# Performance work log

Measured on AMD Instinct MI355X. Metric: run time of the kernel, lower is better.

## Reference

```python
import jax, jax.numpy as jnp
import numpy as np


def setup_inputs() -> dict:
    key = jax.random.key(0)
    ks = jax.random.split(key, 6)
    B, C, H, W, Q = 16, 64, 64, 64, 8192
    HID = 256
    K = C * 9  # 576, unfolded channel count and srnet out_dim (co_mat=1)
    feat = jax.random.normal(ks[0], (B, C, H, W), jnp.float32)
    coord = jax.random.uniform(ks[1], (B, Q, 2), jnp.float32) * 2.0 - 1.0  # normalized [-1,1]
    cell = jnp.ones((B, Q, 2), jnp.float32) * (2.0 / 128.0)  # HR cell size for 128-px grid
    w1 = jax.random.normal(ks[2], (3, HID), jnp.float32) / np.sqrt(3.0)
    b1 = jnp.zeros((HID,), jnp.float32)
    w2 = jax.random.normal(ks[3], (HID, HID), jnp.float32) / np.sqrt(float(HID))
    b2 = jnp.zeros((HID,), jnp.float32)
    w3 = jax.random.normal(ks[4], (HID, K), jnp.float32) / np.sqrt(float(HID))
    b3 = jnp.zeros((K,), jnp.float32)
    return {"feat": feat, "coord": coord, "cell": cell,
            "w1": w1, "b1": b1, "w2": w2, "b2": b2, "w3": w3, "b3": b3}


def reference(feat, coord, cell, w1, b1, w2, b2, w3, b3):
    B, C, H, W = feat.shape
    Q = coord.shape[1]
    K = C * 9
    co_mat = 1
    # F.unfold(feat, 3, padding=1).view(B, C*9, H, W): channel-major, kernel pos minor
    padded = jnp.pad(feat, ((0, 0), (0, 0), (1, 1), (1, 1)))
    patches = jnp.stack([padded[:, :, i:i + H, j:j + W]
                         for i in range(3) for j in range(3)], axis=2)  # [B,C,9,H,W]
    featu = patches.reshape(B, K, H * W)
    # shift query coords by half a cell
    coord_ = coord - cell / 2.0
    coord_q = jnp.clip(coord_ + 1e-6, -1.0 + 1e-6, 1.0 - 1e-6)
    # nearest grid_sample, align_corners=False: idx = round(((c+1)*S - 1)/2)
    # coord[...,0] indexes H (grid y after flip), coord[...,1] indexes W (grid x)
    iy = jnp.clip(jnp.round(((coord_q[..., 0] + 1.0) * H - 1.0) / 2.0), 0, H - 1).astype(jnp.int32)
    ix = jnp.clip(jnp.round(((coord_q[..., 1] + 1.0) * W - 1.0) / 2.0), 0, W - 1).astype(jnp.int32)
    lin = iy * W + ix  # [B,Q]
    q_feat = jnp.take_along_axis(featu, lin[:, None, :], axis=2).transpose(0, 2, 1)  # [B,Q,K]
    # q_coord: make_coord value minus half-pixel shift at the nearest index = 2i/S - 1 (exact)
    qy = 2.0 * iy.astype(jnp.float32) / H - 1.0
    qx = 2.0 * ix.astype(jnp.float32) / W - 1.0
    rel_y = (coord_[..., 0] - qy) * (H / 2.0)
    rel_x = (coord_[..., 1] - qx) * (W / 2.0)
    r_rev = cell[..., 0] * (H / 2.0)
    inp = jnp.stack([rel_y, rel_x, r_rev], axis=-1)  # [B,Q,3]
    # srnet MLP: per-query filter of shape [K, co_mat]
    h = jax.nn.relu(inp @ w1 + b1)
    h = jax.nn.relu(h @ w2 + b2)
    wmat = (h @ w3 + b3).reshape(B, Q, K, co_mat)
    # bmm combine: [1,K] @ [K,co_mat] per query
    pred = jnp.einsum('bqk,bqkc->bqc', q_feat, wmat)  # [B,Q,1]
    return pred
```

## Files before the change

### kernel.cpp

```cpp
#include <hip/hip_runtime.h>
#include <hip/hip_bf16.h>

#define BB 16
#define CC 64
#define HH 64
#define WW 64
#define QQ 8192
#define HID 256
#define KK 576
#define HT 66
#define FROW 264

typedef short short8 __attribute__((ext_vector_type(8)));
typedef short sv4    __attribute__((ext_vector_type(4)));
typedef float f32x4  __attribute__((ext_vector_type(4)));

__device__ __forceinline__ short f2bf(float f) {
    union { float f; unsigned u; } v; v.f = f;
    unsigned r = v.u + 0x7fffu + ((v.u >> 16) & 1u);
    return (short)(r >> 16);
}
__device__ __forceinline__ float bf2f(short s) {
    union { unsigned u; float f; } v; v.u = ((unsigned)(unsigned short)s) << 16;
    return v.f;
}
__device__ __forceinline__ void barrier_lds() {
    asm volatile("s_waitcnt lgkmcnt(0)" ::: "memory");
    __builtin_amdgcn_s_barrier();
    asm volatile("" ::: "memory");
}
__device__ __forceinline__ void glld16(const short* g, short* l) {
    __builtin_amdgcn_global_load_lds(
        (const __attribute__((address_space(1))) void*)g,
        (__attribute__((address_space(3))) void*)l, 16, 0, 0);
}

__global__ __launch_bounds__(256) void prep_transpose_k(const float* __restrict__ feat,
                                                        const float* __restrict__ w2,
                                                        const float* __restrict__ w3,
                                                        const float* __restrict__ b3,
                                                        short* __restrict__ featT,
                                                        short* __restrict__ w3cB,
                                                        short* __restrict__ w2cB) {
    __shared__ float ftile[64][65];
    const int t = threadIdx.x;
    const int gidx = blockIdx.x * 256 + t;

    if (gidx < 156672) {
        int kchunk = gidx / 2176;
        int rem = gidx - kchunk * 2176;
        int n = rem >> 3, j = rem & 7;
        int kglob = kchunk * 8 + j;
        int pos = kglob >> 6, c = kglob & 63;
        float v = 0.f;
        if (n < 256)      v = w3[n * KK + c * 9 + pos];
        else if (n == 256) v = b3[c * 9 + pos];
        w3cB[gidx] = f2bf(v);
    }
    if (gidx < 65536) {
        int kchunk = gidx >> 11;
        int rem = gidx & 2047;
        int n = rem >> 3, j = rem & 7;
        int k = kchunk * 8 + j;
        w2cB[gidx] = f2bf(w2[k * 256 + n]);
    }

    const int b = blockIdx.x / HT;
    const int yy = blockIdx.x - b * HT;
    short* out_row = featT + ((b * HT + yy) * HT) * 64;

    if (yy == 0 || yy == HT - 1) {
        for (int idx = t; idx < HT * 64; idx += 256) out_row[idx] = 0;
        return;
    }
    const int y = yy - 1;
    const float* src = feat + ((b * CC) * HH + y) * WW;
#pragma unroll
    for (int i = 0; i < 16; ++i) {
        int idx = i * 256 + t;
        int c = idx >> 6, x = idx & 63;
        ftile[c][x] = src[c * (HH * WW) + x];
    }
    if (t < 64) out_row[t] = 0;
    else if (t < 128) out_row[(HT - 1) * 64 + (t - 64)] = 0;
    __syncthreads();
#pragma unroll
    for (int i = 0; i < 16; ++i) {
        int idx = i * 256 + t;
        int x = idx >> 6, c = idx & 63;
        out_row[(x + 1) * 64 + c] = f2bf(ftile[c][x]);
    }
}

#define SSTR 72
__global__ __launch_bounds__(256, 2) void conv_k(const short* __restrict__ featT,
                                                 const short* __restrict__ w3cB,
                                                 short* __restrict__ F) {
    __shared__ short slab[3 * HT * SSTR];
    __shared__ short Bb[2][8704];
    const int t = threadIdx.x;
    const int wave = t >> 6, lane = t & 63, quad = lane >> 4, ln16 = lane & 15;
    const int b = blockIdx.x >> 6, y = blockIdx.x & 63;

    f32x4 acc[4][5];
#pragma unroll
    for (int a = 0; a < 4; ++a)
#pragma unroll
        for (int i = 0; i < 5; ++i) acc[a][i] = (f32x4){0.f, 0.f, 0.f, 0.f};

    auto stageB = [&](int buf, int st) {
        const short* src = w3cB + st * 8704;
#pragma unroll
        for (int u = 0; u < 5; ++u) {
            int cidx = (u < 4) ? (u * 4 + wave) : 16;
            if (u < 4 || wave == 0)
                glld16(src + cidx * 512 + lane * 8, &Bb[buf][cidx * 512]);
        }
    };

    stageB(0, 0);

    const short* slabsrc = featT + b * (HT * HT * 64) + y * (HT * 64);
#pragma unroll
    for (int it = 0; it < 7; ++it) {
        int i = it * 256 + t;
        if (i < 1584) {
            short8 v = *(const short8*)(slabsrc + i * 8);
            int row = i >> 3, cs = (i & 7) * 8;
            *(short8*)(&slab[row * SSTR + cs]) = v;
        }
    }
    __syncthreads();

#pragma unroll
    for (int st = 0; st < 18; ++st) {
        const int cur = st & 1;
        if (st < 17) stageB(cur ^ 1, st + 1);
        const int pos = st >> 1, ks = st & 1;
        const int di = pos / 3, dj = pos - di * 3;
        short8 af[4];
#pragma unroll
        for (int ms = 0; ms < 4; ++ms)
            af[ms] = *(const short8*)(&slab[(di * HT + ms * 16 + ln16 + dj) * SSTR + ks * 32 + quad * 8]);
#pragma unroll
        for (int i = 0; i < 5; ++i) {
            int sub = (i < 4) ? (wave + 4 * i) : 16;
            short8 bf = *(const short8*)(&Bb[cur][(quad * 272 + sub * 16 + ln16) * 8]);
#pragma unroll
            for (int ms = 0; ms < 4; ++ms)
                acc[ms][i] = __builtin_amdgcn_mfma_f32_16x16x32_bf16(af[ms], bf, acc[ms][i], 0, 0, 0);
        }
        __syncthreads();
    }

#pragma unroll
    for (int h = 0; h < 2; ++h) {
#pragma unroll
        for (int i = 0; i < 5; ++i) {
            int sub = (i < 4) ? (wave + 4 * i) : 16;
            int n = sub * 16 + ln16;
            bool store = (i < 4) || (wave == 0 && n < FROW);
            if (store) {
#pragma unroll
                for (int ms2 = 0; ms2 < 2; ++ms2) {
                    int ms = h * 2 + ms2;
#pragma unroll
                    for (int r = 0; r < 4; ++r) {
                        int xl = ms2 * 16 + quad * 4 + r;
                        slab[xl * FROW + n] = f2bf(acc[ms][i][r]);
                    }
                }
            }
        }
        __syncthreads();
        short8* dst = (short8*)(F + ((long)(b * 64 + y) * 64 + h * 32) * FROW);
        const short8* src8 = (const short8*)slab;
#pragma unroll
        for (int it = 0; it < 5; ++it) {
            int idx = it * 256 + t;
            if (idx < (32 * FROW) / 8) dst[idx] = src8[idx];
        }
        __syncthreads();
    }
}

#define HSPLIT 136
__global__ __launch_bounds__(256, 2) void mlp_k(const float* __restrict__ coord,
                                                const float* __restrict__ cell,
                                                const float* __restrict__ w1,
                                                const float* __restrict__ b1,
                                                const float* __restrict__ b2v,
                                                const short* __restrict__ w2cB,
                                                const short* __restrict__ F,
                                                float* __restrict__ out) {
    __shared__ short Hh[64 * HSPLIT];
    __shared__ short Wb[2][8192];
    __shared__ float red_s[64][4];

    const int t = threadIdx.x;
    const int wave = t >> 6, lane = t & 63, quad = lane >> 4, ln16 = lane & 15;
    const int qbase = blockIdx.x * 64;
    const int b = qbase >> 13;

    auto stageW = [&](int buf, int s) {
        const short* src = w2cB + s * 8192;
#pragma unroll
        for (int u = 0; u < 4; ++u) {
            int cidx = u * 4 + wave;
            glld16(src + cidx * 512 + lane * 8, &Wb[buf][cidx * 512]);
        }
    };

    stageW(0, 0);

    const int g = qbase + lane;
    const float2 cc = *(const float2*)(coord + g * 2);
    const float2 ce = *(const float2*)(cell + g * 2);
    const float coy = cc.x - ce.x * 0.5f, cox = cc.y - ce.y * 0.5f;
    const float cqy = fminf(fmaxf(coy + 1e-6f, -0.999999f), 0.999999f);
    const float cqx = fminf(fmaxf(cox + 1e-6f, -0.999999f), 0.999999f);
    int iy = (int)rintf(((cqy + 1.0f) * 64.0f - 1.0f) * 0.5f); iy = min(max(iy, 0), 63);
    int ix = (int)rintf(((cqx + 1.0f) * 64.0f - 1.0f) * 0.5f); ix = min(max(ix, 0), 63);
    const int lin = iy * 64 + ix;
    const float in0 = (coy - ((float)iy * (1.0f / 32.0f) - 1.0f)) * 32.0f;
    const float in1 = (cox - ((float)ix * (1.0f / 32.0f) - 1.0f)) * 32.0f;
    const float in2 = ce.x * 32.0f;

    short8 hv[8];
    const int k0w = wave * 64;
#pragma unroll
    for (int c8 = 0; c8 < 8; ++c8) {
        const int k0 = k0w + c8 * 8;
        f32x4 wa0 = *(const f32x4*)(w1 + k0),       wa1 = *(const f32x4*)(w1 + k0 + 4);
        f32x4 wb0 = *(const f32x4*)(w1 + 256 + k0), wb1 = *(const f32x4*)(w1 + 256 + k0 + 4);
        f32x4 wc0 = *(const f32x4*)(w1 + 512 + k0), wc1 = *(const f32x4*)(w1 + 512 + k0 + 4);
        f32x4 bb0 = *(const f32x4*)(b1 + k0),       bb1 = *(const f32x4*)(b1 + k0 + 4);
#pragma unroll
        for (int jj = 0; jj < 4; ++jj) {
            float v0 = fmaf(in0, wa0[jj], fmaf(in1, wb0[jj], fmaf(in2, wc0[jj], bb0[jj])));
            float v1 = fmaf(in0, wa1[jj], fmaf(in1, wb1[jj], fmaf(in2, wc1[jj], bb1[jj])));
            hv[c8][jj]     = f2bf(fmaxf(v0, 0.f));
            hv[c8][jj + 4] = f2bf(fmaxf(v1, 0.f));
        }
    }
    if (wave < 2) {
#pragma unroll
        for (int c8 = 0; c8 < 8; ++c8)
            *(short8*)(&Hh[lane * HSPLIT + wave * 64 + c8 * 8]) = hv[c8];
    }
    f32x4 b2q[4];
#pragma unroll
    for (int i = 0; i < 4; ++i)
        b2q[i] = *(const f32x4*)(b2v + wave * 64 + i * 16 + quad * 4);
    __syncthreads();

    f32x4 acc2[4][4];
#pragma unroll
    for (int i = 0; i < 4; ++i)
#pragma unroll
        for (int ms = 0; ms < 4; ++ms) acc2[i][ms] = (f32x4){0.f, 0.f, 0.f, 0.f};
#pragma unroll
    for (int s = 0; s < 8; ++s) {
        const int cur = s & 1;
        if (s < 7) stageW(cur ^ 1, s + 1);
        short8 wf[4], hf[4];
#pragma unroll
        for (int i = 0; i < 4; ++i)
            wf[i] = *(const short8*)(&Wb[cur][(quad * 256 + wave * 64 + i * 16 + ln16) * 8]);
        const int col = (s & 3) * 32 + quad * 8;
#pragma unroll
        for (int ms = 0; ms < 4; ++ms)
            hf[ms] = *(const short8*)(&Hh[(ms * 16 + ln16) * HSPLIT + col]);
#pragma unroll
        for (int i = 0; i < 4; ++i)
#pragma unroll
            for (int ms = 0; ms < 4; ++ms)
                acc2[i][ms] = __builtin_amdgcn_mfma_f32_16x16x32_bf16(wf[i], hf[ms], acc2[i][ms], 0, 0, 0);
        if (s == 3) {
            __syncthreads();
            if (wave >= 2) {
#pragma unroll
                for (int c8 = 0; c8 < 8; ++c8)
                    *(short8*)(&Hh[lane * HSPLIT + (wave - 2) * 64 + c8 * 8]) = hv[c8];
            }
            barrier_lds();
        } else if (s < 7) {
            __syncthreads();
        }
    }

    const short* Fb = F + (long)b * 4096 * FROW;
    sv4 fv[4][4];
#pragma unroll
    for (int ms = 0; ms < 4; ++ms) {
        int linm = __shfl(lin, ms * 16 + ln16, 64);
        const short* Fr = Fb + (long)linm * FROW + wave * 64 + quad * 4;
#pragma unroll
        for (int i = 0; i < 4; ++i) fv[ms][i] = *(const sv4*)(Fr + i * 16);
    }
    const float fbv = bf2f(Fb[(long)lin * FROW + 256]);

    float part[4] = {0.f, 0.f, 0.f, 0.f};
#pragma unroll
    for (int i = 0; i < 4; ++i)
#pragma unroll
        for (int ms = 0; ms < 4; ++ms)
#pragma unroll
            for (int r = 0; r < 4; ++r)
                part[ms] = fmaf(fmaxf(acc2[i][ms][r] + b2q[i][r], 0.f), bf2f(fv[ms][i][r]), part[ms]);
#pragma unroll
    for (int ms = 0; ms < 4; ++ms) {
        part[ms] += __shfl_xor(part[ms], 16, 64);
        part[ms] += __shfl_xor(part[ms], 32, 64);
    }
    if (quad == 0) {
#pragma unroll
        for (int ms = 0; ms < 4; ++ms) red_s[ms * 16 + ln16][wave] = part[ms];
    }
    barrier_lds();
    if (t < 64)
        out[qbase + t] = red_s[t][0] + red_s[t][1] + red_s[t][2] + red_s[t][3] + fbv;
}

extern "C" void kernel_launch(void* const* d_in, const int* in_sizes, int n_in,
                              void* d_out, int out_size, void* d_ws, size_t ws_size,
                              hipStream_t stream) {
    const float* feat  = (const float*)d_in[0];
    const float* coord = (const float*)d_in[1];
    const float* cell  = (const float*)d_in[2];
    const float* w1    = (const float*)d_in[3];
    const float* b1    = (const float*)d_in[4];
    const float* w2    = (const float*)d_in[5];
    const float* b2    = (const float*)d_in[6];
    const float* w3    = (const float*)d_in[7];
    const float* b3    = (const float*)d_in[8];
    float* out = (float*)d_out;

    char* ws = (char*)d_ws;
    short* w3cB  = (short*)(ws);
    short* w2cB  = (short*)(ws + 313344);
    short* featT = (short*)(ws + 444416);
    short* F     = (short*)(ws + 9365504);
    (void)ws_size; (void)in_sizes; (void)n_in; (void)out_size;

    prep_transpose_k<<<BB * HT, 256, 0, stream>>>(feat, w2, w3, b3, featT, w3cB, w2cB);
    conv_k<<<BB * HH, 256, 0, stream>>>(featT, w3cB, F);
    mlp_k<<<(BB * QQ) / 64, 256, 0, stream>>>(coord, cell, w1, b1, b2, w2cB, F, out);
}
```

Measured before the change: 158.4 us.

## Stream W2 fragments directly into registers and drop LDS weight staging

Removes the double-buffered LDS staging of W2 in the MLP kernel. Each wave now loads its W2 MFMA fragments straight from global memory into a three-slot register ring, prefetched two stages ahead. The full hidden activation is written to LDS once, so the per-stage __syncthreads and the mid-loop second H write go away. The feature gathers and b2 loads move inside the loop to overlap with MFMA work, and launch bounds rise to 3 blocks per SM. The cost is more VGPR pressure and redundant global/L2 weight traffic, since every block reads W2 separately.

```diff
diff --git a/kernel.cpp b/kernel.cpp
--- a/kernel.cpp
+++ b/kernel.cpp
@@ -184,8 +184,8 @@
     }
 }
 
-#define HSPLIT 136
-__global__ __launch_bounds__(256, 2) void mlp_k(const float* __restrict__ coord,
+#define HSTR 264
+__global__ __launch_bounds__(256, 3) void mlp_k(const float* __restrict__ coord,
                                                 const float* __restrict__ cell,
                                                 const float* __restrict__ w1,
                                                 const float* __restrict__ b1,
@@ -193,8 +193,7 @@
                                                 const short* __restrict__ w2cB,
                                                 const short* __restrict__ F,
                                                 float* __restrict__ out) {
-    __shared__ short Hh[64 * HSPLIT];
-    __shared__ short Wb[2][8192];
+    __shared__ short Hh[64 * HSTR];
     __shared__ float red_s[64][4];
 
     const int t = threadIdx.x;
@@ -202,20 +201,21 @@
     const int qbase = blockIdx.x * 64;
     const int b = qbase >> 13;
 
-    auto stageW = [&](int buf, int s) {
-        const short* src = w2cB + s * 8192;
-#pragma unroll
-        for (int u = 0; u < 4; ++u) {
-            int cidx = u * 4 + wave;
-            glld16(src + cidx * 512 + lane * 8, &Wb[buf][cidx * 512]);
-        }
+    short8 wbuf[3][4];
+    const short* w2base = w2cB + (quad * 256 + wave * 64 + ln16) * 8;
+    auto loadW = [&](int s, int slot) {
+#pragma unroll
+        for (int i = 0; i < 4; ++i)
+            wbuf[slot][i] = *(const short8*)(w2base + s * 8192 + i * 128);
     };
-
-    stageW(0, 0);
 
     const int g = qbase + lane;
     const float2 cc = *(const float2*)(coord + g * 2);
     const float2 ce = *(const float2*)(cell + g * 2);
+
+    loadW(0, 0);
+    loadW(1, 1);
+
     const float coy = cc.x - ce.x * 0.5f, cox = cc.y - ce.y * 0.5f;
     const float cqy = fminf(fmaxf(coy + 1e-6f, -0.999999f), 0.999999f);
     const float cqx = fminf(fmaxf(cox + 1e-6f, -0.999999f), 0.999999f);
@@ -226,6 +226,10 @@
     const float in1 = (cox - ((float)ix * (1.0f / 32.0f) - 1.0f)) * 32.0f;
     const float in2 = ce.x * 32.0f;
 
+    int linm[4];
+#pragma unroll
+    for (int ms = 0; ms < 4; ++ms) linm[ms] = __shfl(lin, ms * 16 + ln16, 64);
+
     short8 hv[8];
     const int k0w = wave * 64;
 #pragma unroll
@@ -243,63 +247,50 @@
             hv[c8][jj + 4] = f2bf(fmaxf(v1, 0.f));
         }
     }
-    if (wave < 2) {
-#pragma unroll
-        for (int c8 = 0; c8 < 8; ++c8)
-            *(short8*)(&Hh[lane * HSPLIT + wave * 64 + c8 * 8]) = hv[c8];
-    }
-    f32x4 b2q[4];
-#pragma unroll
-    for (int i = 0; i < 4; ++i)
-        b2q[i] = *(const f32x4*)(b2v + wave * 64 + i * 16 + quad * 4);
-    __syncthreads();
-
-    f32x4 acc2[4][4];
-#pragma unroll
-    for (int i = 0; i < 4; ++i)
-#pragma unroll
-        for (int ms = 0; ms < 4; ++ms) acc2[i][ms] = (f32x4){0.f, 0.f, 0.f, 0.f};
-#pragma unroll
-    for (int s = 0; s < 8; ++s) {
-        const int cur = s & 1;
-        if (s < 7) stageW(cur ^ 1, s + 1);
-        short8 wf[4], hf[4];
-#pragma unroll
-        for (int i = 0; i < 4; ++i)
-            wf[i] = *(const short8*)(&Wb[cur][(quad * 256 + wave * 64 + i * 16 + ln16) * 8]);
-        const int col = (s & 3) * 32 + quad * 8;
-#pragma unroll
-        for (int ms = 0; ms < 4; ++ms)
-            hf[ms] = *(const short8*)(&Hh[(ms * 16 + ln16) * HSPLIT + col]);
-#pragma unroll
-        for (int i = 0; i < 4; ++i)
-#pragma unroll
-            for (int ms = 0; ms < 4; ++ms)
-                acc2[i][ms] = __builtin_amdgcn_mfma_f32_16x16x32_bf16(wf[i], hf[ms], acc2[i][ms], 0, 0, 0);
-        if (s == 3) {
-            __syncthreads();
-            if (wave >= 2) {
-#pragma unroll
-                for (int c8 = 0; c8 < 8; ++c8)
-                    *(short8*)(&Hh[lane * HSPLIT + (wave - 2) * 64 + c8 * 8]) = hv[c8];
-            }
-            barrier_lds();
-        } else if (s < 7) {
-            __syncthreads();
-        }
-    }
+#pragma unroll
+    for (int c8 = 0; c8 < 8; ++c8)
+        *(short8*)(&Hh[lane * HSTR + wave * 64 + c8 * 8]) = hv[c8];
+    barrier_lds();
 
     const short* Fb = F + (long)b * 4096 * FROW;
     sv4 fv[4][4];
-#pragma unroll
-    for (int ms = 0; ms < 4; ++ms) {
-        int linm = __shfl(lin, ms * 16 + ln16, 64);
-        const short* Fr = Fb + (long)linm * FROW + wave * 64 + quad * 4;
-#pragma unroll
-        for (int i = 0; i < 4; ++i) fv[ms][i] = *(const sv4*)(Fr + i * 16);
-    }
-    const float fbv = bf2f(Fb[(long)lin * FROW + 256]);
-
+    short fbs = 0;
+    f32x4 b2q[4];
+    f32x4 acc2[4][4];
+#pragma unroll
+    for (int i = 0; i < 4; ++i)
+#pragma unroll
+        for (int ms = 0; ms < 4; ++ms) acc2[i][ms] = (f32x4){0.f, 0.f, 0.f, 0.f};
+
+#pragma unroll
+    for (int s = 0; s < 8; ++s) {
+        if (s < 6) loadW(s + 2, (s + 2) % 3);
+        short8 hf[4];
+#pragma unroll
+        for (int ms = 0; ms < 4; ++ms)
+            hf[ms] = *(const short8*)(&Hh[(ms * 16 + ln16) * HSTR + s * 32 + quad * 8]);
+        if (s == 6) {
+#pragma unroll
+            for (int ms = 0; ms < 4; ++ms) {
+                const short* Fr = Fb + (long)linm[ms] * FROW + wave * 64 + quad * 4;
+#pragma unroll
+                for (int i = 0; i < 4; ++i) fv[ms][i] = *(const sv4*)(Fr + i * 16);
+            }
+            fbs = Fb[(long)lin * FROW + 256];
+        }
+        if (s == 7) {
+#pragma unroll
+            for (int i = 0; i < 4; ++i)
+                b2q[i] = *(const f32x4*)(b2v + wave * 64 + i * 16 + quad * 4);
+        }
+#pragma unroll
+        for (int i = 0; i < 4; ++i)
+#pragma unroll
+            for (int ms = 0; ms < 4; ++ms)
+                acc2[i][ms] = __builtin_amdgcn_mfma_f32_16x16x32_bf16(wbuf[s % 3][i], hf[ms], acc2[i][ms], 0, 0, 0);
+    }
+
+    const float fbv = bf2f(fbs);
     float part[4] = {0.f, 0.f, 0.f, 0.f};
 #pragma unroll
     for (int i = 0; i < 4; ++i)
```

Result: faster. 150.9 us (-4.7%).
